# Optimization experiments

Hardware: AMD Instinct MI355X
Metric: run time of the kernel (lower is better)

The kernel has to match this reference:

```python
import jax, jax.numpy as jnp
import numpy as np

C = 64
CK = C // 8  # query/key channels

def setup_inputs() -> dict:
    key = jax.random.key(0)
    ks = jax.random.split(key, 8)
    x = jax.random.normal(ks[0], (4, C, 16, 16, 16), dtype=jnp.float32)
    # 1x1x1 Conv3d weights collapse to [out_ch, in_ch] matrices
    wq = jax.random.normal(ks[1], (CK, C), dtype=jnp.float32) * (1.0 / np.sqrt(C))
    bq = jax.random.normal(ks[2], (CK,), dtype=jnp.float32) * 0.01
    wk = jax.random.normal(ks[3], (CK, C), dtype=jnp.float32) * (1.0 / np.sqrt(C))
    bk = jax.random.normal(ks[4], (CK,), dtype=jnp.float32) * 0.01
    wv = jax.random.normal(ks[5], (C, C), dtype=jnp.float32) * (1.0 / np.sqrt(C))
    bv = jax.random.normal(ks[6], (C,), dtype=jnp.float32) * 0.01
    gamma = jnp.ones((1,), dtype=jnp.float32) * 0.5  # nonzero so attention path affects output
    return {"x": x, "wq": wq, "bq": bq, "wk": wk, "bk": bk, "wv": wv, "bv": bv, "gamma": gamma}

def reference(x, wq, bq, wk, bk, wv, bv, gamma):
    B, Cc, D, H, W = x.shape
    N = D * H * W
    xf = x.reshape(B, Cc, N)  # [B, C, N]
    q = jnp.einsum('kc,bcn->bkn', wq, xf) + bq[None, :, None]  # [B, CK, N]
    k = jnp.einsum('kc,bcn->bkn', wk, xf) + bk[None, :, None]  # [B, CK, N]
    v = jnp.einsum('oc,bcn->bon', wv, xf) + bv[None, :, None]  # [B, C, N]
    # energy[b,i,j] = sum_k q[b,k,i] * k[b,k,j]; softmax over j (no scaling, per source)
    energy = jnp.einsum('bki,bkj->bij', q, k)  # [B, N, N]
    attn = jax.nn.softmax(energy, axis=-1)
    # out[b,c,i] = sum_j v[b,c,j] * attn[b,i,j]
    out = jnp.einsum('bcj,bij->bci', v, attn)  # [B, C, N]
    out = out.reshape(B, Cc, D, H, W)
    return gamma * out + x
```

## Files before the change

kernel.cpp:

```cpp
#include <hip/hip_runtime.h>
#include <hip/hip_bf16.h>

#define BATCH  4
#define CDIM   64
#define CKD    8
#define NPOS   4096
#define RLN2   1.44269504f
#define SH2    25.96851039f
#define ECL2   14.42695041f
#define PTP    72

typedef _Float16 f16x8 __attribute__((ext_vector_type(8)));
typedef float    f32x4 __attribute__((ext_vector_type(4)));

__device__ __forceinline__ f16x8 pack8(const float* e) {
    f16x8 v;
#pragma unroll
    for (int i = 0; i < 8; ++i) v[i] = (_Float16)e[i];
    return v;
}

__device__ __forceinline__ void gl_lds16(const void* g, void* l) {
    __builtin_amdgcn_global_load_lds(
        (const __attribute__((address_space(1))) void*)g,
        (__attribute__((address_space(3))) void*)l, 16, 0, 0);
}

__global__ __launch_bounds__(256, 4) void proj_kernel(
    const float* __restrict__ x,
    const float* __restrict__ wq, const float* __restrict__ bq,
    const float* __restrict__ wk, const float* __restrict__ bk,
    const float* __restrict__ wv, const float* __restrict__ bv,
    _Float16* __restrict__ qh, _Float16* __restrict__ kh,
    _Float16* __restrict__ vswz)
{
    __shared__ float red[64 * 73];

    const int bid  = blockIdx.x;
    const int part = bid >> 8;
    const int tid  = threadIdx.x;
    const int s    = tid & 63;
    const int h    = tid >> 6;
    const int pos  = (bid & 255) * 64 + s;
    const int b    = pos >> 12;
    const int n    = pos & 4095;
    const int c0   = part * 16;
    const int cl0  = h * 16;

    const float* xb = x + (size_t)b * CDIM * NPOS + n;

    float vacc[16];
#pragma unroll
    for (int o = 0; o < 16; ++o) vacc[o] = 0.f;
    float qacc[8] = {0.f, 0.f, 0.f, 0.f, 0.f, 0.f, 0.f, 0.f};

    if (part < 2) {
        const float* wqk = (part == 0) ? wq : wk;
#pragma unroll
        for (int cc = 0; cc < 16; ++cc) {
            const int c = cl0 + cc;
            const float xv = xb[(size_t)c * NPOS];
#pragma unroll
            for (int o = 0; o < 8; ++o)  qacc[o] = fmaf(wqk[o * CDIM + c], xv, qacc[o]);
#pragma unroll
            for (int o = 0; o < 16; ++o) vacc[o] = fmaf(wv[(c0 + o) * CDIM + c], xv, vacc[o]);
        }
    } else {
#pragma unroll
        for (int cc = 0; cc < 16; ++cc) {
            const int c = cl0 + cc;
            const float xv = xb[(size_t)c * NPOS];
#pragma unroll
            for (int o = 0; o < 16; ++o) vacc[o] = fmaf(wv[(c0 + o) * CDIM + c], xv, vacc[o]);
        }
    }

    float* rs = red + s * 73;
    if (h != 0) {
        float* rh = rs + (h - 1) * 24;
        if (part < 2) {
#pragma unroll
            for (int i = 0; i < 8; ++i)  rh[i] = qacc[i];
#pragma unroll
            for (int o = 0; o < 16; ++o) rh[8 + o] = vacc[o];
        } else {
#pragma unroll
            for (int o = 0; o < 16; ++o) rh[o] = vacc[o];
        }
    }
    __syncthreads();
    if (h != 0) return;

    if (part < 2) {
#pragma unroll
        for (int i = 0; i < 8; ++i)  qacc[i] += rs[i] + rs[24 + i] + rs[48 + i];
#pragma unroll
        for (int o = 0; o < 16; ++o) vacc[o] += rs[8 + o] + rs[32 + o] + rs[56 + o];

        const float* bqk = (part == 0) ? bq : bk;
        const float scl  = (part == 0) ? RLN2 : 1.0f;
        f16x8 qv;
#pragma unroll
        for (int o = 0; o < 8; ++o) qv[o] = (_Float16)((qacc[o] + bqk[o]) * scl);
        _Float16* dst = ((part == 0) ? qh : kh) + ((size_t)(b * NPOS + n)) * CKD;
        *(f16x8*)dst = qv;
    } else {
#pragma unroll
        for (int o = 0; o < 16; ++o) vacc[o] += rs[o] + rs[24 + o] + rs[48 + o];
    }

    const int jq = (n >> 2) & 3;
    const int ju = ((n >> 4) & 1) * 4 + (n & 3);
    const size_t vbase = (size_t)(b * 128 + (n >> 5)) * 2048 + jq * 8 + ju;
#pragma unroll
    for (int o = 0; o < 16; ++o)
        vswz[vbase + (size_t)(c0 + o) * 32] = (_Float16)(vacc[o] + bv[c0 + o]);
}

template<int NSPLIT>
__global__ __launch_bounds__(256, 4) void attn_kernel(
    const _Float16* __restrict__ qh, const _Float16* __restrict__ kh,
    const _Float16* __restrict__ vswz,
    __hip_bfloat16* __restrict__ po, float* __restrict__ pl)
{
    constexpr int JCHUNK = NPOS / NSPLIT;
    constexpr int NIT64  = JCHUNK / 64;

    __shared__ __align__(16) _Float16 vbuf[2][4096];
    __shared__ __hip_bfloat16 pt[4][16][PTP];

    const int bid   = blockIdx.x;
    const int split = bid & (NSPLIT - 1);
    const int itile = (bid / NSPLIT) & 31;
    const int b     = bid / (NSPLIT * 32);
    const int tid   = threadIdx.x;
    const int wave  = tid >> 6;
    const int lane  = tid & 63;
    const int quad  = lane >> 4;
    const int m16   = lane & 15;

    const int i0 = itile * 128 + wave * 32;

    f16x8 qa0 = *(const f16x8*)(qh + ((size_t)(b * NPOS + i0 + m16)) * CKD);
    f16x8 qa1 = *(const f16x8*)(qh + ((size_t)(b * NPOS + i0 + 16 + m16)) * CKD);
    if (quad != 0) { qa0 = (f16x8){}; qa1 = (f16x8){}; }

    const _Float16* kp = kh + ((size_t)(b * NPOS + split * JCHUNK) + (size_t)m16) * CKD;

    const _Float16* vsrc = vswz + (size_t)b * 262144
                         + (size_t)split * (JCHUNK / 32) * 2048
                         + wave * 1024 + lane * 8;

    f32x4 acc0[4], acc1[4];
#pragma unroll
    for (int nb = 0; nb < 4; ++nb) {
        acc0[nb] = (f32x4){0.f, 0.f, 0.f, 0.f};
        acc1[nb] = (f32x4){0.f, 0.f, 0.f, 0.f};
    }
    float ls0 = 0.f, ls1 = 0.f;
    const f32x4 csh = {-SH2, -SH2, -SH2, -SH2};

    gl_lds16(vsrc,       &vbuf[0][wave * 1024]);
    gl_lds16(vsrc + 512, &vbuf[0][wave * 1024 + 512]);
    asm volatile("s_waitcnt vmcnt(0)" ::: "memory");
    __builtin_amdgcn_s_barrier();

    int cur = 0;
    for (int it = 0; it < NIT64; ++it) {
        {
            const _Float16* vn = vsrc + (size_t)(it + 1) * 4096;
            gl_lds16(vn,       &vbuf[cur ^ 1][wave * 1024]);
            gl_lds16(vn + 512, &vbuf[cur ^ 1][wave * 1024 + 512]);
        }

#pragma unroll
        for (int h = 0; h < 2; ++h) {
            const f16x8 kfa = *(const f16x8*)(kp + (size_t)(h * 32) * CKD);
            const f16x8 kfb = *(const f16x8*)(kp + (size_t)(h * 32 + 16) * CKD);

            __builtin_amdgcn_s_setprio(1);
            const f32x4 s0a = __builtin_amdgcn_mfma_f32_16x16x32_f16(kfa, qa0, csh, 0, 0, 0);
            const f32x4 s0b = __builtin_amdgcn_mfma_f32_16x16x32_f16(kfb, qa0, csh, 0, 0, 0);
            const f32x4 s1a = __builtin_amdgcn_mfma_f32_16x16x32_f16(kfa, qa1, csh, 0, 0, 0);
            const f32x4 s1b = __builtin_amdgcn_mfma_f32_16x16x32_f16(kfb, qa1, csh, 0, 0, 0);
            __builtin_amdgcn_s_setprio(0);

            float e0[8], e1[8];
#pragma unroll
            for (int r = 0; r < 4; ++r) {
                e0[r]     = __builtin_exp2f(fminf(s0a[r], ECL2));
                e0[4 + r] = __builtin_exp2f(fminf(s0b[r], ECL2));
                e1[r]     = __builtin_exp2f(fminf(s1a[r], ECL2));
                e1[4 + r] = __builtin_exp2f(fminf(s1b[r], ECL2));
            }
            ls0 += ((e0[0] + e0[1]) + (e0[2] + e0[3])) + ((e0[4] + e0[5]) + (e0[6] + e0[7]));
            ls1 += ((e1[0] + e1[1]) + (e1[2] + e1[3])) + ((e1[4] + e1[5]) + (e1[6] + e1[7]));

            const f16x8 pa0 = pack8(e0);
            const f16x8 pa1 = pack8(e1);

            __builtin_amdgcn_s_setprio(1);
#pragma unroll
            for (int nb = 0; nb < 4; ++nb) {
                const f16x8 vb = *(const f16x8*)(&vbuf[cur][h * 2048 + m16 * 32 + quad * 8 + nb * 512]);
                acc0[nb] = __builtin_amdgcn_mfma_f32_16x16x32_f16(pa0, vb, acc0[nb], 0, 0, 0);
                acc1[nb] = __builtin_amdgcn_mfma_f32_16x16x32_f16(pa1, vb, acc1[nb], 0, 0, 0);
            }
            __builtin_amdgcn_s_setprio(0);
        }
        kp += 64 * CKD;

        asm volatile("s_waitcnt vmcnt(0)" ::: "memory");
        __builtin_amdgcn_s_barrier();
        cur ^= 1;
    }

    ls0 += __shfl_xor(ls0, 16);
    ls0 += __shfl_xor(ls0, 32);
    ls1 += __shfl_xor(ls1, 16);
    ls1 += __shfl_xor(ls1, 32);

    const int sbx = split * BATCH + b;
    if (quad == 0) {
        pl[(size_t)sbx * NPOS + i0 + m16]      = ls0;
        pl[(size_t)sbx * NPOS + i0 + 16 + m16] = ls1;
    }

    __hip_bfloat16* ept = &pt[wave][0][0];

#define EPILOG(ACC, IOFS)                                                     \
    do {                                                                      \
        _Pragma("unroll")                                                     \
        for (int nb = 0; nb < 4; ++nb)                                        \
            _Pragma("unroll")                                                 \
            for (int r = 0; r < 4; ++r)                                       \
                ept[(quad * 4 + r) * PTP + nb * 16 + m16] =                   \
                    __float2bfloat16(ACC[nb][r]);                             \
        _Pragma("unroll")                                                     \
        for (int g2 = 0; g2 < 16; ++g2) {                                     \
            const int c = quad + g2 * 4;                                      \
            po[((size_t)sbx * CDIM + c) * NPOS + i0 + (IOFS) + m16] =         \
                ept[m16 * PTP + c];                                           \
        }                                                                     \
    } while (0)

    EPILOG(acc0, 0);
    EPILOG(acc1, 16);
#undef EPILOG
}

template<int NSPLIT>
__global__ __launch_bounds__(256) void combine_kernel(
    const float* __restrict__ x,
    const __hip_bfloat16* __restrict__ po, const float* __restrict__ pl,
    const float* __restrict__ gamma, float* __restrict__ out)
{
    const int t  = blockIdx.x * 256 + threadIdx.x;
    const int i4 = (t & 1023) * 4;
    const int c  = (t >> 10) & 63;
    const int b  = t >> 16;

    const unsigned short* pou = (const unsigned short*)po;

    float L0 = 0.f, L1 = 0.f, L2 = 0.f, L3 = 0.f;
    float O0 = 0.f, O1 = 0.f, O2 = 0.f, O3 = 0.f;
#pragma unroll
    for (int s = 0; s < NSPLIT; ++s) {
        const size_t sb = (size_t)(s * BATCH + b);
        const float4 lv = *(const float4*)(pl + sb * NPOS + i4);
        const ushort4 pv = *(const ushort4*)(pou + (sb * CDIM + c) * NPOS + i4);
        L0 += lv.x; L1 += lv.y; L2 += lv.z; L3 += lv.w;
        O0 += __uint_as_float((unsigned)pv.x << 16);
        O1 += __uint_as_float((unsigned)pv.y << 16);
        O2 += __uint_as_float((unsigned)pv.z << 16);
        O3 += __uint_as_float((unsigned)pv.w << 16);
    }
    const float g = gamma[0];
    const size_t xi = ((size_t)(b * CDIM + c)) * NPOS + i4;
    const float4 xv = *(const float4*)(x + xi);
    float4 o;
    o.x = fmaf(g, O0 / L0, xv.x);
    o.y = fmaf(g, O1 / L1, xv.y);
    o.z = fmaf(g, O2 / L2, xv.z);
    o.w = fmaf(g, O3 / L3, xv.w);
    *(float4*)(out + xi) = o;
}

extern "C" void kernel_launch(void* const* d_in, const int* in_sizes, int n_in,
                              void* d_out, int out_size, void* d_ws, size_t ws_size,
                              hipStream_t stream)
{
    const float* x     = (const float*)d_in[0];
    const float* wq    = (const float*)d_in[1];
    const float* bq    = (const float*)d_in[2];
    const float* wk    = (const float*)d_in[3];
    const float* bk    = (const float*)d_in[4];
    const float* wv    = (const float*)d_in[5];
    const float* bv    = (const float*)d_in[6];
    const float* gamma = (const float*)d_in[7];
    float* out = (float*)d_out;

    char* ws = (char*)d_ws;
    _Float16*       qh   = (_Float16*)(ws);
    _Float16*       kh   = (_Float16*)(ws + (256 << 10));
    _Float16*       vswz = (_Float16*)(ws + (512 << 10));
    __hip_bfloat16* po   = (__hip_bfloat16*)(ws + (2560 << 10));

    const size_t po8_end = (2560ull << 10) + 8ull * 4 * CDIM * NPOS * 2;
    const size_t need8   = po8_end + 8ull * 4 * NPOS * 4;

    proj_kernel<<<1024, 256, 0, stream>>>(x, wq, bq, wk, bk, wv, bv, qh, kh, vswz);

    if (ws_size >= need8) {
        float* pl = (float*)(ws + po8_end);
        attn_kernel<8><<<BATCH * 32 * 8, 256, 0, stream>>>(qh, kh, vswz, po, pl);
        combine_kernel<8><<<1024, 256, 0, stream>>>(x, po, pl, gamma, out);
    } else {
        const size_t po4_end = (2560ull << 10) + 4ull * 4 * CDIM * NPOS * 2;
        float* pl = (float*)(ws + po4_end);
        attn_kernel<4><<<BATCH * 32 * 4, 256, 0, stream>>>(qh, kh, vswz, po, pl);
        combine_kernel<4><<<1024, 256, 0, stream>>>(x, po, pl, gamma, out);
    }
}
```

Baseline: 122.6 us.

## Triple-buffer V and stage K through LDS with async global-to-LDS loads

Moves from double-buffered V to a three-stage LDS ring, prefetching two iterations ahead. K tiles are now also staged into LDS with 4-byte global_load_lds instead of being read directly from global memory per iteration. The barrier moves to the loop top with a partial vmcnt wait, so loads for later iterations can stay in flight while the current tile is computed. The cost is more LDS per block, which may lower occupancy, and correctness depends on the vmcnt count matching the number of outstanding loads. The tail iterations prefetch past the chunk end, possibly reading out of bounds on the last split.

```diff
diff --git a/kernel.cpp b/kernel.cpp
--- a/kernel.cpp
+++ b/kernel.cpp
@@ -24,6 +24,11 @@
     __builtin_amdgcn_global_load_lds(
         (const __attribute__((address_space(1))) void*)g,
         (__attribute__((address_space(3))) void*)l, 16, 0, 0);
+}
+__device__ __forceinline__ void gl_lds4(const void* g, void* l) {
+    __builtin_amdgcn_global_load_lds(
+        (const __attribute__((address_space(1))) void*)g,
+        (__attribute__((address_space(3))) void*)l, 4, 0, 0);
 }
 
 __global__ __launch_bounds__(256, 4) void proj_kernel(
@@ -126,7 +131,8 @@
     constexpr int JCHUNK = NPOS / NSPLIT;
     constexpr int NIT64  = JCHUNK / 64;
 
-    __shared__ __align__(16) _Float16 vbuf[2][4096];
+    __shared__ __align__(16) _Float16 vbuf[3][4096];
+    __shared__ __align__(16) _Float16 kbuf[3][512];
     __shared__ __hip_bfloat16 pt[4][16][PTP];
 
     const int bid   = blockIdx.x;
@@ -145,11 +151,11 @@
     f16x8 qa1 = *(const f16x8*)(qh + ((size_t)(b * NPOS + i0 + 16 + m16)) * CKD);
     if (quad != 0) { qa0 = (f16x8){}; qa1 = (f16x8){}; }
 
-    const _Float16* kp = kh + ((size_t)(b * NPOS + split * JCHUNK) + (size_t)m16) * CKD;
-
     const _Float16* vsrc = vswz + (size_t)b * 262144
                          + (size_t)split * (JCHUNK / 32) * 2048
                          + wave * 1024 + lane * 8;
+    const _Float16* ksrc = kh + ((size_t)(b * NPOS + split * JCHUNK)) * CKD
+                         + wave * 128 + lane * 2;
 
     f32x4 acc0[4], acc1[4];
 #pragma unroll
@@ -160,23 +166,33 @@
     float ls0 = 0.f, ls1 = 0.f;
     const f32x4 csh = {-SH2, -SH2, -SH2, -SH2};
 
-    gl_lds16(vsrc,       &vbuf[0][wave * 1024]);
-    gl_lds16(vsrc + 512, &vbuf[0][wave * 1024 + 512]);
-    asm volatile("s_waitcnt vmcnt(0)" ::: "memory");
-    __builtin_amdgcn_s_barrier();
+    gl_lds16(vsrc,              &vbuf[0][wave * 1024]);
+    gl_lds16(vsrc + 512,        &vbuf[0][wave * 1024 + 512]);
+    gl_lds4 (ksrc,              &kbuf[0][wave * 128]);
+    gl_lds16(vsrc + 4096,       &vbuf[1][wave * 1024]);
+    gl_lds16(vsrc + 4096 + 512, &vbuf[1][wave * 1024 + 512]);
+    gl_lds4 (ksrc + 512,        &kbuf[1][wave * 128]);
 
     int cur = 0;
     for (int it = 0; it < NIT64; ++it) {
+        asm volatile("s_waitcnt vmcnt(3)" ::: "memory");
+        __builtin_amdgcn_s_barrier();
+
+        const int nx2 = (cur == 0) ? 2 : cur - 1;
         {
-            const _Float16* vn = vsrc + (size_t)(it + 1) * 4096;
-            gl_lds16(vn,       &vbuf[cur ^ 1][wave * 1024]);
-            gl_lds16(vn + 512, &vbuf[cur ^ 1][wave * 1024 + 512]);
-        }
+            const _Float16* vn = vsrc + (size_t)(it + 2) * 4096;
+            gl_lds16(vn,       &vbuf[nx2][wave * 1024]);
+            gl_lds16(vn + 512, &vbuf[nx2][wave * 1024 + 512]);
+            gl_lds4(ksrc + (size_t)(it + 2) * 512, &kbuf[nx2][wave * 128]);
+        }
+
+        const _Float16* kb = &kbuf[cur][0];
+        const _Float16* vb0 = &vbuf[cur][0];
 
 #pragma unroll
         for (int h = 0; h < 2; ++h) {
-            const f16x8 kfa = *(const f16x8*)(kp + (size_t)(h * 32) * CKD);
-            const f16x8 kfb = *(const f16x8*)(kp + (size_t)(h * 32 + 16) * CKD);
+            const f16x8 kfa = *(const f16x8*)(kb + h * 256 + m16 * 8);
+            const f16x8 kfb = *(const f16x8*)(kb + h * 256 + 128 + m16 * 8);
 
             __builtin_amdgcn_s_setprio(1);
             const f32x4 s0a = __builtin_amdgcn_mfma_f32_16x16x32_f16(kfa, qa0, csh, 0, 0, 0);
@@ -202,17 +218,13 @@
             __builtin_amdgcn_s_setprio(1);
 #pragma unroll
             for (int nb = 0; nb < 4; ++nb) {
-                const f16x8 vb = *(const f16x8*)(&vbuf[cur][h * 2048 + m16 * 32 + quad * 8 + nb * 512]);
+                const f16x8 vb = *(const f16x8*)(vb0 + h * 2048 + m16 * 32 + quad * 8 + nb * 512);
                 acc0[nb] = __builtin_amdgcn_mfma_f32_16x16x32_f16(pa0, vb, acc0[nb], 0, 0, 0);
                 acc1[nb] = __builtin_amdgcn_mfma_f32_16x16x32_f16(pa1, vb, acc1[nb], 0, 0, 0);
             }
             __builtin_amdgcn_s_setprio(0);
         }
-        kp += 64 * CKD;
-
-        asm volatile("s_waitcnt vmcnt(0)" ::: "memory");
-        __builtin_amdgcn_s_barrier();
-        cur ^= 1;
+        cur = (cur == 2) ? 0 : cur + 1;
     }
 
     ls0 += __shfl_xor(ls0, 16);
```

Result: no change. 123.5 us (+0.7%).
